# Optimization experiments

Measured on AMD Instinct MI355X. Metric: run time of the kernel, lower is better.

## Reference

```python
import jax, jax.numpy as jnp
import numpy as np

HEADS = 4
ATTN_MODE = 'strided'
LOCAL_ATTN_CTX = 32
BLOCKSIZE = 32


def strided_transpose(x, n_ctx, local_attn_ctx):
    # [n, t, e] -> [n, bT_ctx, local, e] -> [n, local, bT_ctx, e] -> [n, t, e]
    bT_ctx = n_ctx // local_attn_ctx
    n, t, e = x.shape
    x = x.reshape(n, bT_ctx, local_attn_ctx, e)
    x = jnp.transpose(x, (0, 2, 1, 3))
    return x.reshape(n, t, e)


def setup_inputs() -> dict:
    key = jax.random.key(0)
    kq, kk, kv = jax.random.split(key, 3)
    shape = (2, 4096, 1024)
    return {
        'q': jax.random.normal(kq, shape, dtype=jnp.float32),
        'k': jax.random.normal(kk, shape, dtype=jnp.float32),
        'v': jax.random.normal(kv, shape, dtype=jnp.float32),
    }


def reference(q, k, v):
    n_ctx = q.shape[1]
    if ATTN_MODE == 'strided':
        bT_ctx = n_ctx // LOCAL_ATTN_CTX
        assert bT_ctx % BLOCKSIZE == 0
        q = strided_transpose(q, n_ctx, LOCAL_ATTN_CTX)
        k = strided_transpose(k, n_ctx, LOCAL_ATTN_CTX)
        v = strided_transpose(v, n_ctx, LOCAL_ATTN_CTX)
    n_state = q.shape[-1] // HEADS
    scale = 1.0 / np.sqrt(n_state)
    w = jnp.einsum('nte,nse->nts', q, k)            # [n, t, t] full scores
    w = jax.nn.softmax(w * scale, axis=-1)
    a = jnp.einsum('nts,nse->nte', w, v)
    if ATTN_MODE == 'strided':
        n, t, e = a.shape
        bT_ctx = n_ctx // LOCAL_ATTN_CTX
        a = a.reshape(n, LOCAL_ATTN_CTX, bT_ctx, e)
        a = jnp.transpose(a, (0, 2, 1, 3))
        a = a.reshape(n, t, e)
    return a
```

## Files before the change

kernel.cpp:

```cpp
#include <hip/hip_runtime.h>

using short8  = __attribute__((ext_vector_type(8))) short;
using ushort8 = __attribute__((ext_vector_type(8))) unsigned short;
using f32x4   = __attribute__((ext_vector_type(4))) float;

#define T 4096
#define E 1024
#define NB 2
#define BK 32

__device__ __forceinline__ unsigned short f2bf(float f) {
    unsigned int u = __builtin_bit_cast(unsigned int, f);
    u = (u + 0x7FFFu + ((u >> 16) & 1u)) >> 16;
    return (unsigned short)u;
}

__device__ __forceinline__ void gld16(const unsigned short* g, unsigned short* l) {
    __builtin_amdgcn_global_load_lds(
        (__attribute__((address_space(1))) void*)g,
        (__attribute__((address_space(3))) void*)l, 16, 0, 0);
}

__device__ __forceinline__ void do_cvt(const float* __restrict__ src,
                                       unsigned short* __restrict__ dst, int blk) {
    size_t i = ((size_t)blk * 256 + threadIdx.x) * 8;
    float4 f0 = *(const float4*)(src + i);
    float4 f1 = *(const float4*)(src + i + 4);
    ushort8 u;
    u[0]=f2bf(f0.x); u[1]=f2bf(f0.y); u[2]=f2bf(f0.z); u[3]=f2bf(f0.w);
    u[4]=f2bf(f1.x); u[5]=f2bf(f1.y); u[6]=f2bf(f1.z); u[7]=f2bf(f1.w);
    *(ushort8*)(dst + i) = u;
}

__device__ __forceinline__ void do_vt(const float* __restrict__ v,
                                      unsigned short* __restrict__ vt, int id,
                                      float (*tile)[65]) {
    int b   = id / (64 * 16);
    int rem = id % (64 * 16);
    int t0  = (rem / 16) * 64;
    int e0  = (rem % 16) * 64;
    int tid = threadIdx.x;
    int r   = tid >> 2;
    int c0  = (tid & 3) * 16;
    const float* src = v + ((size_t)(b * T + t0 + r)) * E + e0 + c0;
    #pragma unroll
    for (int i = 0; i < 4; i++) {
        float4 f = *(const float4*)(src + i * 4);
        tile[r][c0 + i*4 + 0] = f.x;
        tile[r][c0 + i*4 + 1] = f.y;
        tile[r][c0 + i*4 + 2] = f.z;
        tile[r][c0 + i*4 + 3] = f.w;
    }
    __syncthreads();
    int er = tid >> 2;
    #pragma unroll
    for (int ch = 0; ch < 2; ch++) {
        int tl = (tid & 3) * 16 + ch * 8;
        ushort8 u;
        #pragma unroll
        for (int j = 0; j < 8; j++) u[j] = f2bf(tile[tl + j][er]);
        *(ushort8*)(vt + ((size_t)(b * E + e0 + er)) * T + t0 + tl) = u;
    }
}

__global__ __launch_bounds__(256) void prep(const float* __restrict__ q,
                                            const float* __restrict__ k,
                                            const float* __restrict__ v,
                                            unsigned short* __restrict__ qb,
                                            unsigned short* __restrict__ kb,
                                            unsigned short* __restrict__ vt,
                                            float* __restrict__ lsum) {
    __shared__ float tile[64][65];
    int bid = blockIdx.x;
    if (bid < 4096)        do_cvt(q, qb, bid);
    else if (bid < 8192)   do_cvt(k, kb, bid - 4096);
    else if (bid < 10240)  do_vt(v, vt, bid - 8192, tile);
    else                   lsum[(bid - 10240) * 256 + threadIdx.x] = 0.0f;
}

__global__ __launch_bounds__(256) void prologue(const float* __restrict__ q,
                                                const float* __restrict__ k,
                                                unsigned short* __restrict__ qb,
                                                unsigned short* __restrict__ kb,
                                                float* __restrict__ lsum) {
    int bid = blockIdx.x;
    if (bid < 4096)      do_cvt(q, qb, bid);
    else if (bid < 8192) do_cvt(k, kb, bid - 4096);
    else                 lsum[(bid - 8192) * 256 + threadIdx.x] = 0.0f;
}
__global__ __launch_bounds__(256) void v_transpose(const float* __restrict__ v,
                                                   unsigned short* __restrict__ vt) {
    __shared__ float tile[64][65];
    do_vt(v, vt, blockIdx.x, tile);
}

__global__ __launch_bounds__(512, 2) void pass1(const unsigned short* __restrict__ qb,
                                                const unsigned short* __restrict__ kb,
                                                unsigned short* __restrict__ P,
                                                float* __restrict__ lsum) {
    constexpr int TW = 256 * BK;
    __shared__ unsigned short ldsA[3 * TW];
    __shared__ unsigned short ldsB[3 * TW];

    const int bx = blockIdx.x;
    const int x = bx & 7, j = bx >> 3;
    const int gm = x * 4 + (j & 3);
    const int nt = j >> 2;
    const int b = gm >> 4, mt = gm & 15;
    const int tid = threadIdx.x;
    const int lane = tid & 63, wave = tid >> 6;
    const int l15 = lane & 15, kq = lane >> 4;
    const int wm = (wave & 1) * 128, wn = (wave >> 1) * 64;

    const unsigned short* Ab = qb + ((size_t)b * T + mt * 256) * E;
    const unsigned short* Bb = kb + ((size_t)b * T + nt * 256) * E;

    const unsigned short* ga[2]; const unsigned short* gb[2]; int lo[2];
    #pragma unroll
    for (int i = 0; i < 2; i++) {
        int p = i * 512 + tid;
        int r = p >> 2;
        int qs = (p & 3) ^ ((p >> 3) & 3);
        ga[i] = Ab + (size_t)r * E + qs * 8;
        gb[i] = Bb + (size_t)r * E + qs * 8;
        lo[i] = (i * 512 + wave * 64) * 8;
    }
    int aoff[8], boff[4];
    #pragma unroll
    for (int mi = 0; mi < 8; mi++) { int r = wm + mi * 16 + l15; aoff[mi] = (r * 4 + (kq ^ ((r >> 1) & 3))) * 8; }
    #pragma unroll
    for (int ni = 0; ni < 4; ni++) { int r = wn + ni * 16 + l15; boff[ni] = (r * 4 + (kq ^ ((r >> 1) & 3))) * 8; }

    f32x4 acc[8][4];
    #pragma unroll
    for (int i = 0; i < 8; i++)
        #pragma unroll
        for (int jj = 0; jj < 4; jj++) acc[i][jj] = {};

    #pragma unroll
    for (int t = 0; t < 2; t++) {
        gld16(ga[0] + t * BK, ldsA + t * TW + lo[0]);
        gld16(ga[1] + t * BK, ldsA + t * TW + lo[1]);
        gld16(gb[0] + t * BK, ldsB + t * TW + lo[0]);
        gld16(gb[1] + t * BK, ldsB + t * TW + lo[1]);
    }

    int c = 0, p2 = 2, pk = 2;
    for (int kt = 0; kt < E / BK; kt++) {
        gld16(ga[0] + pk * BK, ldsA + p2 * TW + lo[0]);
        gld16(ga[1] + pk * BK, ldsA + p2 * TW + lo[1]);
        asm volatile("s_waitcnt vmcnt(6)" ::: "memory");
        asm volatile("s_barrier" ::: "memory");

        const unsigned short* A = ldsA + c * TW;
        const unsigned short* B = ldsB + c * TW;
        short8 af[4], bf[4];
        #pragma unroll
        for (int i = 0; i < 4; i++) {
            af[i] = *(const short8*)(A + aoff[i]);
            bf[i] = *(const short8*)(B + boff[i]);
        }
        __builtin_amdgcn_s_setprio(1);
        #pragma unroll
        for (int mi = 0; mi < 4; mi++)
            #pragma unroll
            for (int ni = 0; ni < 4; ni++)
                acc[mi][ni] = __builtin_amdgcn_mfma_f32_16x16x32_bf16(af[mi], bf[ni], acc[mi][ni], 0, 0, 0);
        __builtin_amdgcn_s_setprio(0);
        asm volatile("s_barrier" ::: "memory");

        gld16(gb[0] + pk * BK, ldsB + p2 * TW + lo[0]);
        gld16(gb[1] + pk * BK, ldsB + p2 * TW + lo[1]);
        short8 af2[4];
        #pragma unroll
        for (int i = 0; i < 4; i++) af2[i] = *(const short8*)(A + aoff[4 + i]);
        __builtin_amdgcn_s_setprio(1);
        #pragma unroll
        for (int mi = 0; mi < 4; mi++)
            #pragma unroll
            for (int ni = 0; ni < 4; ni++)
                acc[4 + mi][ni] = __builtin_amdgcn_mfma_f32_16x16x32_bf16(af2[mi], bf[ni], acc[4 + mi][ni], 0, 0, 0);
        __builtin_amdgcn_s_setprio(0);
        asm volatile("s_barrier" ::: "memory");

        if (++c == 3) c = 0;
        if (++p2 == 3) p2 = 0;
        if (++pk == E / BK) pk = 0;
    }

    const int quad = lane >> 4;
    const float sl2 = 0.0625f * 1.44269504089f;
    const int col0 = nt * 256 + wn + l15;
    #pragma unroll
    for (int mi = 0; mi < 8; mi++) {
        #pragma unroll
        for (int r = 0; r < 4; r++) {
            int row = mt * 256 + wm + mi * 16 + quad * 4 + r;
            size_t base = ((size_t)b * T + row) * T + col0;
            float s = 0.0f;
            #pragma unroll
            for (int ni = 0; ni < 4; ni++) {
                float p = exp2f(acc[mi][ni][r] * sl2 - 12.0f);
                P[base + ni * 16] = f2bf(p);
                s += p;
            }
            s += __shfl_xor(s, 1);
            s += __shfl_xor(s, 2);
            s += __shfl_xor(s, 4);
            s += __shfl_xor(s, 8);
            if (l15 == 0) atomicAdd(lsum + b * T + row, s);
        }
    }
}

__global__ __launch_bounds__(512, 2) void pass2(const unsigned short* __restrict__ P,
                                                const unsigned short* __restrict__ vt,
                                                const float* __restrict__ lsum,
                                                float* __restrict__ out) {
    constexpr int TWA = 256 * BK;
    constexpr int TWB = 128 * BK;
    __shared__ unsigned short ldsA[3 * TWA];
    __shared__ unsigned short ldsB[3 * TWB];

    const int bx = blockIdx.x;
    const int x = bx & 7, j = bx >> 3;
    const int gm = x * 4 + (j & 3);
    const int nt = j >> 2;
    const int b = gm >> 4, mt = gm & 15;
    const int tid = threadIdx.x;
    const int lane = tid & 63, wave = tid >> 6;
    const int l15 = lane & 15, kq = lane >> 4;
    const int wm = (wave & 3) * 64, wn = (wave >> 2) * 64;

    const unsigned short* Ab = P + ((size_t)b * T + mt * 256) * T;
    const unsigned short* Bb = vt + ((size_t)b * E + nt * 128) * T;

    const unsigned short* ga[2]; int lao[2];
    #pragma unroll
    for (int i = 0; i < 2; i++) {
        int p = i * 512 + tid;
        int r = p >> 2;
        int qs = (p & 3) ^ ((p >> 3) & 3);
        ga[i] = Ab + (size_t)r * T + qs * 8;
        lao[i] = (i * 512 + wave * 64) * 8;
    }
    const unsigned short* gb; int lbo;
    {
        int p = tid;
        int r = p >> 2;
        int qs = (p & 3) ^ ((p >> 3) & 3);
        gb = Bb + (size_t)r * T + qs * 8;
        lbo = (wave * 64) * 8;
    }
    int aoff[4], boff[4];
    #pragma unroll
    for (int mi = 0; mi < 4; mi++) { int r = wm + mi * 16 + l15; aoff[mi] = (r * 4 + (kq ^ ((r >> 1) & 3))) * 8; }
    #pragma unroll
    for (int ni = 0; ni < 4; ni++) { int r = wn + ni * 16 + l15; boff[ni] = (r * 4 + (kq ^ ((r >> 1) & 3))) * 8; }

    f32x4 acc[4][4];
    #pragma unroll
    for (int i = 0; i < 4; i++)
        #pragma unroll
        for (int jj = 0; jj < 4; jj++) acc[i][jj] = {};

    #pragma unroll
    for (int t = 0; t < 2; t++) {
        gld16(ga[0] + t * BK, ldsA + t * TWA + lao[0]);
        gld16(ga[1] + t * BK, ldsA + t * TWA + lao[1]);
        gld16(gb    + t * BK, ldsB + t * TWB + lbo);
    }

    int c = 0, p2 = 2, pk = 2;
    for (int kt = 0; kt < T / BK; kt++) {
        gld16(ga[0] + pk * BK, ldsA + p2 * TWA + lao[0]);
        gld16(ga[1] + pk * BK, ldsA + p2 * TWA + lao[1]);
        gld16(gb    + pk * BK, ldsB + p2 * TWB + lbo);
        asm volatile("s_waitcnt vmcnt(6)" ::: "memory");
        asm volatile("s_barrier" ::: "memory");

        const unsigned short* A = ldsA + c * TWA;
        const unsigned short* B = ldsB + c * TWB;
        short8 af[4], bf[4];
        #pragma unroll
        for (int i = 0; i < 4; i++) {
            af[i] = *(const short8*)(A + aoff[i]);
            bf[i] = *(const short8*)(B + boff[i]);
        }
        __builtin_amdgcn_s_setprio(1);
        #pragma unroll
        for (int mi = 0; mi < 4; mi++)
            #pragma unroll
            for (int ni = 0; ni < 4; ni++)
                acc[mi][ni] = __builtin_amdgcn_mfma_f32_16x16x32_bf16(af[mi], bf[ni], acc[mi][ni], 0, 0, 0);
        __builtin_amdgcn_s_setprio(0);
        asm volatile("s_barrier" ::: "memory");

        if (++c == 3) c = 0;
        if (++p2 == 3) p2 = 0;
        if (++pk == T / BK) pk = 0;
    }

    const int quad = lane >> 4;
    const int col0 = nt * 128 + wn + l15;
    #pragma unroll
    for (int mi = 0; mi < 4; mi++) {
        #pragma unroll
        for (int r = 0; r < 4; r++) {
            int row = mt * 256 + wm + mi * 16 + quad * 4 + r;
            float rl = 1.0f / lsum[b * T + row];
            size_t base = ((size_t)b * T + row) * E + col0;
            #pragma unroll
            for (int ni = 0; ni < 4; ni++)
                out[base + ni * 16] = acc[mi][ni][r] * rl;
        }
    }
}

extern "C" void kernel_launch(void* const* d_in, const int* in_sizes, int n_in,
                              void* d_out, int out_size, void* d_ws, size_t ws_size,
                              hipStream_t stream) {
    const float* q = (const float*)d_in[0];
    const float* k = (const float*)d_in[1];
    const float* v = (const float*)d_in[2];
    float* out = (float*)d_out;

    const size_t QK = (size_t)NB * T * E;
    const size_t PSZ = (size_t)NB * T * T;
    float* lsum = (float*)d_ws;
    unsigned short* qbw = (unsigned short*)((char*)d_ws + 32768);
    unsigned short* kbw = qbw + QK;
    unsigned short* Pw  = kbw + QK;

    const size_t full_need = 32768 + (3 * QK + PSZ) * sizeof(unsigned short);

    if (ws_size >= full_need) {
        unsigned short* vtw = Pw + PSZ;
        prep<<<10272, 256, 0, stream>>>(q, k, v, qbw, kbw, vtw, lsum);
        pass1<<<512, 512, 0, stream>>>(qbw, kbw, Pw, lsum);
        pass2<<<256, 512, 0, stream>>>(Pw, vtw, lsum, out);
    } else {
        unsigned short* vtw = qbw;
        prologue<<<8224, 256, 0, stream>>>(q, k, qbw, kbw, lsum);
        pass1<<<512, 512, 0, stream>>>(qbw, kbw, Pw, lsum);
        v_transpose<<<NB * 64 * 16, 256, 0, stream>>>(v, vtw);
        pass2<<<256, 512, 0, stream>>>(Pw, vtw, lsum, out);
    }
}
```

Measured before the change: 329.9 us.

## Restructure GEMM main loops into 4-stage LDS pipeline with interleaved loads and MFMA phases

Both GEMM passes are rewritten from a 3-buffer ring with runtime modulo counters into a statically unrolled 4-stage LDS pipeline. Each k-slab is processed in phases that issue the next global-to-LDS loads and then wait on vmcnt only every other slab. LDS fragment reads are issued before the barrier and guarded with lgkmcnt(0) so they overlap the prefetch. LDS use grows to four stages, and launch bounds drop to one block per SM, so occupancy falls in exchange for deeper prefetch and fewer waits.

```diff
diff --git a/kernel.cpp b/kernel.cpp
--- a/kernel.cpp
+++ b/kernel.cpp
@@ -7,7 +7,6 @@
 #define T 4096
 #define E 1024
 #define NB 2
-#define BK 32
 
 __device__ __forceinline__ unsigned short f2bf(float f) {
     unsigned int u = __builtin_bit_cast(unsigned int, f);
@@ -94,13 +93,35 @@
     do_vt(v, vt, blockIdx.x, tile);
 }
 
-__global__ __launch_bounds__(512, 2) void pass1(const unsigned short* __restrict__ qb,
+#define P1_PHASE(S, MH, LB, STAGE, GATE) do {                                   \
+    const unsigned short* A_ = ldsA + (S) * 8192;                               \
+    short8 af[4];                                                               \
+    _Pragma("unroll") for (int i_ = 0; i_ < 4; i_++)                            \
+        af[i_] = *(const short8*)(A_ + aoff[(MH)*4 + i_]);                      \
+    if (LB) {                                                                   \
+        const unsigned short* B_ = ldsB + (S) * 8192;                           \
+        _Pragma("unroll") for (int i_ = 0; i_ < 4; i_++)                        \
+            bf[i_] = *(const short8*)(B_ + boff[i_]);                           \
+    }                                                                           \
+    STAGE                                                                       \
+    GATE                                                                        \
+    asm volatile("s_barrier" ::: "memory");                                     \
+    asm volatile("s_waitcnt lgkmcnt(0)" ::: "memory");                          \
+    __builtin_amdgcn_s_setprio(1);                                              \
+    _Pragma("unroll") for (int mi_ = 0; mi_ < 4; mi_++)                         \
+        _Pragma("unroll") for (int ni_ = 0; ni_ < 4; ni_++)                     \
+            acc[(MH)*4 + mi_][ni_] = __builtin_amdgcn_mfma_f32_16x16x32_bf16(   \
+                af[mi_], bf[ni_], acc[(MH)*4 + mi_][ni_], 0, 0, 0);             \
+    __builtin_amdgcn_s_setprio(0);                                              \
+    asm volatile("s_barrier" ::: "memory");                                     \
+} while (0)
+
+__global__ __launch_bounds__(512, 1) void pass1(const unsigned short* __restrict__ qb,
                                                 const unsigned short* __restrict__ kb,
                                                 unsigned short* __restrict__ P,
                                                 float* __restrict__ lsum) {
-    constexpr int TW = 256 * BK;
-    __shared__ unsigned short ldsA[3 * TW];
-    __shared__ unsigned short ldsB[3 * TW];
+    __shared__ unsigned short ldsA[4 * 8192];
+    __shared__ unsigned short ldsB[4 * 8192];
 
     const int bx = blockIdx.x;
     const int x = bx & 7, j = bx >> 3;
@@ -115,21 +136,21 @@
     const unsigned short* Ab = qb + ((size_t)b * T + mt * 256) * E;
     const unsigned short* Bb = kb + ((size_t)b * T + nt * 256) * E;
 
-    const unsigned short* ga[2]; const unsigned short* gb[2]; int lo[2];
+    const unsigned short* aS[2]; const unsigned short* bS[2]; int lo[2];
     #pragma unroll
     for (int i = 0; i < 2; i++) {
         int p = i * 512 + tid;
-        int r = p >> 2;
-        int qs = (p & 3) ^ ((p >> 3) & 3);
-        ga[i] = Ab + (size_t)r * E + qs * 8;
-        gb[i] = Bb + (size_t)r * E + qs * 8;
+        int r = p >> 2, c = p & 3;
+        int sw = (c ^ ((r >> 1) & 3)) * 8;
+        aS[i] = Ab + (size_t)r * E + sw;
+        bS[i] = Bb + (size_t)r * E + sw;
         lo[i] = (i * 512 + wave * 64) * 8;
     }
     int aoff[8], boff[4];
     #pragma unroll
-    for (int mi = 0; mi < 8; mi++) { int r = wm + mi * 16 + l15; aoff[mi] = (r * 4 + (kq ^ ((r >> 1) & 3))) * 8; }
-    #pragma unroll
-    for (int ni = 0; ni < 4; ni++) { int r = wn + ni * 16 + l15; boff[ni] = (r * 4 + (kq ^ ((r >> 1) & 3))) * 8; }
+    for (int mf = 0; mf < 8; mf++) { int r = wm + mf * 16 + l15; aoff[mf] = (r * 4 + (kq ^ ((r >> 1) & 3))) * 8; }
+    #pragma unroll
+    for (int nf = 0; nf < 4; nf++) { int r = wn + nf * 16 + l15; boff[nf] = (r * 4 + (kq ^ ((r >> 1) & 3))) * 8; }
 
     f32x4 acc[8][4];
     #pragma unroll
@@ -137,70 +158,46 @@
         #pragma unroll
         for (int jj = 0; jj < 4; jj++) acc[i][jj] = {};
 
-    #pragma unroll
-    for (int t = 0; t < 2; t++) {
-        gld16(ga[0] + t * BK, ldsA + t * TW + lo[0]);
-        gld16(ga[1] + t * BK, ldsA + t * TW + lo[1]);
-        gld16(gb[0] + t * BK, ldsB + t * TW + lo[0]);
-        gld16(gb[1] + t * BK, ldsB + t * TW + lo[1]);
-    }
-
-    int c = 0, p2 = 2, pk = 2;
-    for (int kt = 0; kt < E / BK; kt++) {
-        gld16(ga[0] + pk * BK, ldsA + p2 * TW + lo[0]);
-        gld16(ga[1] + pk * BK, ldsA + p2 * TW + lo[1]);
-        asm volatile("s_waitcnt vmcnt(6)" ::: "memory");
-        asm volatile("s_barrier" ::: "memory");
-
-        const unsigned short* A = ldsA + c * TW;
-        const unsigned short* B = ldsB + c * TW;
-        short8 af[4], bf[4];
-        #pragma unroll
-        for (int i = 0; i < 4; i++) {
-            af[i] = *(const short8*)(A + aoff[i]);
-            bf[i] = *(const short8*)(B + boff[i]);
-        }
-        __builtin_amdgcn_s_setprio(1);
-        #pragma unroll
-        for (int mi = 0; mi < 4; mi++)
-            #pragma unroll
-            for (int ni = 0; ni < 4; ni++)
-                acc[mi][ni] = __builtin_amdgcn_mfma_f32_16x16x32_bf16(af[mi], bf[ni], acc[mi][ni], 0, 0, 0);
-        __builtin_amdgcn_s_setprio(0);
-        asm volatile("s_barrier" ::: "memory");
-
-        gld16(gb[0] + pk * BK, ldsB + p2 * TW + lo[0]);
-        gld16(gb[1] + pk * BK, ldsB + p2 * TW + lo[1]);
-        short8 af2[4];
-        #pragma unroll
-        for (int i = 0; i < 4; i++) af2[i] = *(const short8*)(A + aoff[4 + i]);
-        __builtin_amdgcn_s_setprio(1);
-        #pragma unroll
-        for (int mi = 0; mi < 4; mi++)
-            #pragma unroll
-            for (int ni = 0; ni < 4; ni++)
-                acc[4 + mi][ni] = __builtin_amdgcn_mfma_f32_16x16x32_bf16(af2[mi], bf[ni], acc[4 + mi][ni], 0, 0, 0);
-        __builtin_amdgcn_s_setprio(0);
-        asm volatile("s_barrier" ::: "memory");
-
-        if (++c == 3) c = 0;
-        if (++p2 == 3) p2 = 0;
-        if (++pk == E / BK) pk = 0;
-    }
+    gld16(aS[0] + 0,  ldsA + 0 * 8192 + lo[0]);  gld16(aS[1] + 0,  ldsA + 0 * 8192 + lo[1]);
+    gld16(bS[0] + 0,  ldsB + 0 * 8192 + lo[0]);  gld16(bS[1] + 0,  ldsB + 0 * 8192 + lo[1]);
+    gld16(aS[0] + 32, ldsA + 1 * 8192 + lo[0]);  gld16(aS[1] + 32, ldsA + 1 * 8192 + lo[1]);
+    gld16(bS[0] + 32, ldsB + 1 * 8192 + lo[0]);  gld16(bS[1] + 32, ldsB + 1 * 8192 + lo[1]);
+    gld16(aS[0] + 64, ldsA + 2 * 8192 + lo[0]);  gld16(aS[1] + 64, ldsA + 2 * 8192 + lo[1]);
+    gld16(bS[0] + 64, ldsB + 2 * 8192 + lo[0]);  gld16(bS[1] + 64, ldsB + 2 * 8192 + lo[1]);
+    asm volatile("s_waitcnt vmcnt(4)" ::: "memory");
+    asm volatile("s_barrier" ::: "memory");
+
+    short8 bf[4];
+    for (int t = 0; t < 8; t++) {
+        const int k1 = (((2 * t + 1) & 15) << 6) + 32;
+        const int k2 = (((2 * t + 2) & 15) << 6);
+        const int k3 = (((2 * t + 3) & 15) << 6);
+        P1_PHASE(0, 0, 1, { gld16(aS[0]+k1, ldsA+3*8192+lo[0]); gld16(aS[1]+k1, ldsA+3*8192+lo[1]); }, ;);
+        P1_PHASE(0, 1, 0, { gld16(bS[0]+k1, ldsB+3*8192+lo[0]); gld16(bS[1]+k1, ldsB+3*8192+lo[1]); }, ;);
+        P1_PHASE(1, 0, 1, { gld16(aS[0]+k2, ldsA+0*8192+lo[0]); gld16(aS[1]+k2, ldsA+0*8192+lo[1]); }, ;);
+        P1_PHASE(1, 1, 0, { gld16(bS[0]+k2, ldsB+0*8192+lo[0]); gld16(bS[1]+k2, ldsB+0*8192+lo[1]); },
+                 asm volatile("s_waitcnt vmcnt(4)" ::: "memory"););
+        P1_PHASE(2, 0, 1, { gld16(aS[0]+k2+32, ldsA+1*8192+lo[0]); gld16(aS[1]+k2+32, ldsA+1*8192+lo[1]); }, ;);
+        P1_PHASE(2, 1, 0, { gld16(bS[0]+k2+32, ldsB+1*8192+lo[0]); gld16(bS[1]+k2+32, ldsB+1*8192+lo[1]); }, ;);
+        P1_PHASE(3, 0, 1, { gld16(aS[0]+k3, ldsA+2*8192+lo[0]); gld16(aS[1]+k3, ldsA+2*8192+lo[1]); }, ;);
+        P1_PHASE(3, 1, 0, { gld16(bS[0]+k3, ldsB+2*8192+lo[0]); gld16(bS[1]+k3, ldsB+2*8192+lo[1]); },
+                 asm volatile("s_waitcnt vmcnt(4)" ::: "memory"););
+    }
+    asm volatile("s_waitcnt vmcnt(0)" ::: "memory");
 
     const int quad = lane >> 4;
     const float sl2 = 0.0625f * 1.44269504089f;
     const int col0 = nt * 256 + wn + l15;
     #pragma unroll
-    for (int mi = 0; mi < 8; mi++) {
+    for (int mf = 0; mf < 8; mf++) {
         #pragma unroll
         for (int r = 0; r < 4; r++) {
-            int row = mt * 256 + wm + mi * 16 + quad * 4 + r;
+            int row = mt * 256 + wm + mf * 16 + quad * 4 + r;
             size_t base = ((size_t)b * T + row) * T + col0;
             float s = 0.0f;
             #pragma unroll
             for (int ni = 0; ni < 4; ni++) {
-                float p = exp2f(acc[mi][ni][r] * sl2 - 12.0f);
+                float p = exp2f(acc[mf][ni][r] * sl2 - 12.0f);
                 P[base + ni * 16] = f2bf(p);
                 s += p;
             }
@@ -213,14 +210,33 @@
     }
 }
 
-__global__ __launch_bounds__(512, 2) void pass2(const unsigned short* __restrict__ P,
+#define P2_PHASE(S, STAGE, GATE) do {                                           \
+    const unsigned short* A_ = ldsA + (S) * 8192;                               \
+    const unsigned short* B_ = ldsB + (S) * 4096;                               \
+    short8 af[4], bf[4];                                                        \
+    _Pragma("unroll") for (int i_ = 0; i_ < 4; i_++) {                          \
+        af[i_] = *(const short8*)(A_ + aoff[i_]);                               \
+        bf[i_] = *(const short8*)(B_ + boff[i_]);                               \
+    }                                                                           \
+    STAGE                                                                       \
+    GATE                                                                        \
+    asm volatile("s_barrier" ::: "memory");                                     \
+    asm volatile("s_waitcnt lgkmcnt(0)" ::: "memory");                          \
+    __builtin_amdgcn_s_setprio(1);                                              \
+    _Pragma("unroll") for (int mi_ = 0; mi_ < 4; mi_++)                         \
+        _Pragma("unroll") for (int ni_ = 0; ni_ < 4; ni_++)                     \
+            acc[mi_][ni_] = __builtin_amdgcn_mfma_f32_16x16x32_bf16(            \
+                af[mi_], bf[ni_], acc[mi_][ni_], 0, 0, 0);                      \
+    __builtin_amdgcn_s_setprio(0);                                              \
+    asm volatile("s_barrier" ::: "memory");                                     \
+} while (0)
+
+__global__ __launch_bounds__(512, 1) void pass2(const unsigned short* __restrict__ P,
                                                 const unsigned short* __restrict__ vt,
                                                 const float* __restrict__ lsum,
                                                 float* __restrict__ out) {
-    constexpr int TWA = 256 * BK;
-    constexpr int TWB = 128 * BK;
-    __shared__ unsigned short ldsA[3 * TWA];
-    __shared__ unsigned short ldsB[3 * TWB];
+    __shared__ unsigned short ldsA[4 * 8192];
+    __shared__ unsigned short ldsB[4 * 4096];
 
     const int bx = blockIdx.x;
     const int x = bx & 7, j = bx >> 3;
@@ -235,28 +251,28 @@
     const unsigned short* Ab = P + ((size_t)b * T + mt * 256) * T;
     const unsigned short* Bb = vt + ((size_t)b * E + nt * 128) * T;
 
-    const unsigned short* ga[2]; int lao[2];
+    const unsigned short* aS[2]; int lo[2];
     #pragma unroll
     for (int i = 0; i < 2; i++) {
         int p = i * 512 + tid;
-        int r = p >> 2;
-        int qs = (p & 3) ^ ((p >> 3) & 3);
-        ga[i] = Ab + (size_t)r * T + qs * 8;
-        lao[i] = (i * 512 + wave * 64) * 8;
-    }
-    const unsigned short* gb; int lbo;
+        int r = p >> 2, c = p & 3;
+        int sw = (c ^ ((r >> 1) & 3)) * 8;
+        aS[i] = Ab + (size_t)r * T + sw;
+        lo[i] = (i * 512 + wave * 64) * 8;
+    }
+    const unsigned short* bS; int lob;
     {
         int p = tid;
-        int r = p >> 2;
-        int qs = (p & 3) ^ ((p >> 3) & 3);
-        gb = Bb + (size_t)r * T + qs * 8;
-        lbo = (wave * 64) * 8;
+        int r = p >> 2, c = p & 3;
+        int sw = (c ^ ((r >> 1) & 3)) * 8;
+        bS = Bb + (size_t)r * T + sw;
+        lob = (wave * 64) * 8;
     }
     int aoff[4], boff[4];
     #pragma unroll
-    for (int mi = 0; mi < 4; mi++) { int r = wm + mi * 16 + l15; aoff[mi] = (r * 4 + (kq ^ ((r >> 1) & 3))) * 8; }
-    #pragma unroll
-    for (int ni = 0; ni < 4; ni++) { int r = wn + ni * 16 + l15; boff[ni] = (r * 4 + (kq ^ ((r >> 1) & 3))) * 8; }
+    for (int mf = 0; mf < 4; mf++) { int r = wm + mf * 16 + l15; aoff[mf] = (r * 4 + (kq ^ ((r >> 1) & 3))) * 8; }
+    #pragma unroll
+    for (int nf = 0; nf < 4; nf++) { int r = wn + nf * 16 + l15; boff[nf] = (r * 4 + (kq ^ ((r >> 1) & 3))) * 8; }
 
     f32x4 acc[4][4];
     #pragma unroll
@@ -264,55 +280,44 @@
         #pragma unroll
         for (int jj = 0; jj < 4; jj++) acc[i][jj] = {};
 
-    #pragma unroll
-    for (int t = 0; t < 2; t++) {
-        gld16(ga[0] + t * BK, ldsA + t * TWA + lao[0]);
-        gld16(ga[1] + t * BK, ldsA + t * TWA + lao[1]);
-        gld16(gb    + t * BK, ldsB + t * TWB + lbo);
-    }
-
-    int c = 0, p2 = 2, pk = 2;
-    for (int kt = 0; kt < T / BK; kt++) {
-        gld16(ga[0] + pk * BK, ldsA + p2 * TWA + lao[0]);
-        gld16(ga[1] + pk * BK, ldsA + p2 * TWA + lao[1]);
-        gld16(gb    + pk * BK, ldsB + p2 * TWB + lbo);
-        asm volatile("s_waitcnt vmcnt(6)" ::: "memory");
-        asm volatile("s_barrier" ::: "memory");
-
-        const unsigned short* A = ldsA + c * TWA;
-        const unsigned short* B = ldsB + c * TWB;
-        short8 af[4], bf[4];
-        #pragma unroll
-        for (int i = 0; i < 4; i++) {
-            af[i] = *(const short8*)(A + aoff[i]);
-            bf[i] = *(const short8*)(B + boff[i]);
-        }
-        __builtin_amdgcn_s_setprio(1);
-        #pragma unroll
-        for (int mi = 0; mi < 4; mi++)
-            #pragma unroll
-            for (int ni = 0; ni < 4; ni++)
-                acc[mi][ni] = __builtin_amdgcn_mfma_f32_16x16x32_bf16(af[mi], bf[ni], acc[mi][ni], 0, 0, 0);
-        __builtin_amdgcn_s_setprio(0);
-        asm volatile("s_barrier" ::: "memory");
-
-        if (++c == 3) c = 0;
-        if (++p2 == 3) p2 = 0;
-        if (++pk == T / BK) pk = 0;
-    }
+    gld16(aS[0] + 0,  ldsA + 0 * 8192 + lo[0]);  gld16(aS[1] + 0,  ldsA + 0 * 8192 + lo[1]);
+    gld16(bS + 0,  ldsB + 0 * 4096 + lob);
+    gld16(aS[0] + 32, ldsA + 1 * 8192 + lo[0]);  gld16(aS[1] + 32, ldsA + 1 * 8192 + lo[1]);
+    gld16(bS + 32, ldsB + 1 * 4096 + lob);
+    gld16(aS[0] + 64, ldsA + 2 * 8192 + lo[0]);  gld16(aS[1] + 64, ldsA + 2 * 8192 + lo[1]);
+    gld16(bS + 64, ldsB + 2 * 4096 + lob);
+    asm volatile("s_waitcnt vmcnt(3)" ::: "memory");
+    asm volatile("s_barrier" ::: "memory");
+
+    for (int t = 0; t < 32; t++) {
+        const int k1 = (((2 * t + 1) & 63) << 6) + 32;
+        const int k2 = (((2 * t + 2) & 63) << 6);
+        const int k3 = (((2 * t + 3) & 63) << 6);
+        P2_PHASE(0, { gld16(aS[0]+k1, ldsA+3*8192+lo[0]); gld16(aS[1]+k1, ldsA+3*8192+lo[1]);
+                      gld16(bS+k1, ldsB+3*4096+lob); }, ;);
+        P2_PHASE(1, { gld16(aS[0]+k2, ldsA+0*8192+lo[0]); gld16(aS[1]+k2, ldsA+0*8192+lo[1]);
+                      gld16(bS+k2, ldsB+0*4096+lob); },
+                 asm volatile("s_waitcnt vmcnt(3)" ::: "memory"););
+        P2_PHASE(2, { gld16(aS[0]+k2+32, ldsA+1*8192+lo[0]); gld16(aS[1]+k2+32, ldsA+1*8192+lo[1]);
+                      gld16(bS+k2+32, ldsB+1*4096+lob); }, ;);
+        P2_PHASE(3, { gld16(aS[0]+k3, ldsA+2*8192+lo[0]); gld16(aS[1]+k3, ldsA+2*8192+lo[1]);
+                      gld16(bS+k3, ldsB+2*4096+lob); },
+                 asm volatile("s_waitcnt vmcnt(3)" ::: "memory"););
+    }
+    asm volatile("s_waitcnt vmcnt(0)" ::: "memory");
 
     const int quad = lane >> 4;
     const int col0 = nt * 128 + wn + l15;
     #pragma unroll
-    for (int mi = 0; mi < 4; mi++) {
+    for (int mf = 0; mf < 4; mf++) {
         #pragma unroll
         for (int r = 0; r < 4; r++) {
-            int row = mt * 256 + wm + mi * 16 + quad * 4 + r;
+            int row = mt * 256 + wm + mf * 16 + quad * 4 + r;
             float rl = 1.0f / lsum[b * T + row];
             size_t base = ((size_t)b * T + row) * E + col0;
             #pragma unroll
             for (int ni = 0; ni < 4; ni++)
-                out[base + ni * 16] = acc[mi][ni][r] * rl;
+                out[base + ni * 16] = acc[mf][ni][r] * rl;
         }
     }
 }
```

After: 292.8 us. 1.13x faster.
